# Performance work log

Measured on AMD Instinct MI355X. Metric: run time of the kernel, lower is better.

Reference implementation:

```python
import jax, jax.numpy as jnp
import numpy as np

BS = 128          # batch size (baked into trans_bs = Linear(bs, 1))
SEQ = 100         # raw seq len; InnerComp concat doubles it to 200
D = 64            # user/item embedding dim
HID = 128         # predictor hidden dim
NITEM = 1000000   # item vocab
NNEG = 99         # negative samples (test mode)
TH1 = 0.007       # InnerComp threshold (~1/BS)
TH2 = 0.007       # InterComp threshold


def setup_inputs() -> dict:
    key = jax.random.key(0)
    ks = list(jax.random.split(key, 40))
    def nrm(i, shape, s=0.05):
        return jax.random.normal(ks[i], shape, jnp.float32) * s
    inp = {
        "u_node": jax.random.randint(ks[0], (BS,), 0, NITEM),
        "i_node": jax.random.randint(ks[1], (BS,), 0, NITEM),
        "neg_samples": jax.random.randint(ks[2], (BS, NNEG), 0, NITEM),
        "seq_d1": jax.random.randint(ks[3], (BS, SEQ), 0, NITEM),
        "seq_d2": jax.random.randint(ks[4], (BS, SEQ), 0, NITEM),
        "long_tail_mask_d1": jax.random.randint(ks[5], (BS, SEQ), 0, 2),
        "long_tail_mask_d2": jax.random.randint(ks[6], (BS, SEQ), 0, 2),
        "emb": nrm(7, (NITEM, D)),
    }
    j = 8
    for name in ["inc1", "inc2", "itc1", "itc2"]:
        inp[name + "_Wnn"] = nrm(j, (D, D)); j += 1
        inp[name + "_bnn"] = nrm(j, (D,)); j += 1
        inp[name + "_Wbs"] = nrm(j, (1, BS)); j += 1
        inp[name + "_bbs"] = nrm(j, (1,)); j += 1
    for name in ["gru1", "gru2"]:
        inp[name + "_Wih"] = nrm(j, (3 * D, D)); j += 1
        inp[name + "_Whh"] = nrm(j, (3 * D, D)); j += 1
        inp[name + "_bih"] = nrm(j, (3 * D,)); j += 1
        inp[name + "_bhh"] = nrm(j, (3 * D,)); j += 1
    inp["fc1_W"] = nrm(j, (HID, 2 * D)); j += 1
    inp["fc1_b"] = nrm(j, (HID,)); j += 1
    inp["fc2_W"] = nrm(j, (1, HID)); j += 1
    inp["fc2_b"] = nrm(j, (1,)); j += 1
    return inp


def _comp(seq_self, seq_other, Wnn, bnn, Wbs, bbs, th):
    # Faithful collapse of InnerComp/InterComp: in the torch code,
    # group_bool[i,j] = max(seq_self[j] @ seq_other[j]^T) is independent of i,
    # and so is the trans_bs output. Same math, no O(bs^2 L^2) blowup.
    g = jnp.max(jnp.einsum('bld,bmd->blm', seq_self, seq_other), axis=(1, 2))  # [bs]
    m = (jax.nn.softmax(g) > th).astype(seq_self.dtype)                        # [bs]
    y = (seq_other * m[:, None, None]) @ Wnn.T + bnn                           # [bs,L,d]
    z = jnp.einsum('j,jld->ld', Wbs[0], y) + bbs[0]                            # [L,d]
    z = jnp.broadcast_to(z[None], seq_self.shape)
    return jnp.concatenate([seq_self, z], axis=1)                              # [bs,2L,d]


def _gru(x, Wih, Whh, bih, bhh):
    # torch.nn.GRU, 1 layer, batch_first, h0 = 0. Gate order: r, z, n.
    B, L, _ = x.shape
    H = Whh.shape[1]
    xp = x @ Wih.T + bih  # [B,L,3H] precomputed input projections
    def step(h, xt):
        gh = h @ Whh.T + bhh
        xr, xz, xn = jnp.split(xt, 3, axis=-1)
        hr, hz, hn = jnp.split(gh, 3, axis=-1)
        r = jax.nn.sigmoid(xr + hr)
        z = jax.nn.sigmoid(xz + hz)
        n = jnp.tanh(xn + r * hn)
        hnew = (1 - z) * n + z * h
        return hnew, hnew
    h0 = jnp.zeros((B, H), x.dtype)
    _, hs = jax.lax.scan(step, h0, jnp.swapaxes(xp, 0, 1))
    return jnp.swapaxes(hs, 0, 1)  # [B,L,H]


def reference(u_node, i_node, neg_samples, seq_d1, seq_d2,
              long_tail_mask_d1, long_tail_mask_d2, emb,
              inc1_Wnn, inc1_bnn, inc1_Wbs, inc1_bbs,
              inc2_Wnn, inc2_bnn, inc2_Wbs, inc2_bbs,
              itc1_Wnn, itc1_bnn, itc1_Wbs, itc1_bbs,
              itc2_Wnn, itc2_bnn, itc2_Wbs, itc2_bbs,
              gru1_Wih, gru1_Whh, gru1_bih, gru1_bhh,
              gru2_Wih, gru2_Whh, gru2_bih, gru2_bhh,
              fc1_W, fc1_b, fc2_W, fc2_b):
    i_feat = emb[i_node][:, None, :]     # [bs,1,d]
    neg_feat = emb[neg_samples]          # [bs,99,d]
    s1 = emb[seq_d1]                     # [bs,SEQ,d]
    s2 = emb[seq_d2]
    # InnerComp (self-comparison), doubles seq len
    s1 = _comp(s1, s1, inc1_Wnn, inc1_bnn, inc1_Wbs, inc1_bbs, TH1)
    s2 = _comp(s2, s2, inc2_Wnn, inc2_bnn, inc2_Wbs, inc2_bbs, TH1)
    # GRU per domain
    s1 = _gru(s1, gru1_Wih, gru1_Whh, gru1_bih, gru1_bhh)
    s2 = _gru(s2, gru2_Wih, gru2_Whh, gru2_bih, gru2_bhh)
    # InterComp (cross-domain), doubles seq len again
    s1n = _comp(s1, s2, itc1_Wnn, itc1_bnn, itc1_Wbs, itc1_bbs, TH2)
    s2n = _comp(s2, s1, itc2_Wnn, itc2_bnn, itc2_Wbs, itc2_bbs, TH2)
    u1 = jnp.mean(s1n, axis=1)           # [bs,d]
    u2 = jnp.mean(s2n, axis=1)
    i_all = jnp.concatenate([i_feat, neg_feat], axis=1)  # [bs,100,d]
    def pred(u):
        c = jnp.concatenate([jnp.broadcast_to(u[:, None, :], i_all.shape), i_all], axis=-1)
        h = jax.nn.relu(c @ fc1_W.T + fc1_b)
        return jax.nn.sigmoid(h @ fc2_W.T + fc2_b)[..., 0]  # [bs,100]
    return pred(u1), pred(u2)
```

## Files before the change

kernel.cpp:

```cpp
#include <hip/hip_runtime.h>
#include <hip/hip_bf16.h>
#include <cstdint>
#include <cstddef>

#define TH 0.007f

#define OFF_S1RAW   0u
#define OFF_S2RAW   819200u
#define OFF_IALL    1638400u
#define OFF_GRU1O   2457600u
#define OFF_GRU2O   4096000u
#define OFF_XP1     5734400u
#define OFF_XP2     8192000u
#define OFF_ZP1     10649600u
#define OFF_ZP2     10668800u
#define OFF_ZINC1   10688000u
#define OFF_ZINC2   10694400u
#define OFF_ZITC1   10700800u
#define OFF_ZITC2   10713600u
#define OFF_G3      10726400u
#define OFF_U1      10727300u
#define OFF_U2      10735492u

__device__ __forceinline__ float sigf(float x) { return 1.0f / (1.0f + __expf(-x)); }
__device__ __forceinline__ float tanhf_(float x) { return 1.0f - 2.0f / (__expf(2.0f * x) + 1.0f); }

__global__ void k_gather(const int* __restrict__ i_node, const int* __restrict__ neg,
                         const int* __restrict__ seq1, const int* __restrict__ seq2,
                         const float* __restrict__ emb, float* __restrict__ ws) {
  int tid = threadIdx.x;
  int r = blockIdx.x * 4 + (tid >> 6);
  int d = tid & 63;
  long idx;
  float* dst;
  if (r < 12800) {
    idx = seq1[r];
    dst = ws + OFF_S1RAW + (size_t)r * 64;
  } else if (r < 25600) {
    int rr = r - 12800;
    idx = seq2[rr];
    dst = ws + OFF_S2RAW + (size_t)rr * 64;
  } else {
    int rr = r - 25600;
    int b = rr / 100, i = rr % 100;
    idx = (i == 0) ? i_node[b] : neg[b * 99 + i - 1];
    dst = ws + OFF_IALL + (size_t)rr * 64;
  }
  dst[d] = emb[idx * 64 + d];
}

__global__ __launch_bounds__(256) void k_gmax(const float* __restrict__ A0, const float* __restrict__ B0, float* g0,
                                              const float* __restrict__ A1, const float* __restrict__ B1, float* g1,
                                              int L, int nbhalf) {
  int half = blockIdx.x / nbhalf;
  int b = blockIdx.x % nbhalf;
  const float* A = half ? A1 : A0;
  const float* B = half ? B1 : B0;
  float* gout = half ? g1 : g0;
  __shared__ __align__(16) float SA[64 * 104];
  __shared__ __align__(16) float SB[64 * 104];
  __shared__ float red[4];
  int tid = threadIdx.x;
  int nch = L / 100;
  float gm = -1e30f;
  for (int ai = 0; ai < nch; ++ai) {
    for (int bi = 0; bi < nch; ++bi) {
      __syncthreads();
      for (int e = tid; e < 6400; e += 256) {
        int l = e >> 6, k = e & 63;
        SA[k * 104 + l] = A[((size_t)b * L + ai * 100 + l) * 64 + k];
        SB[k * 104 + l] = B[((size_t)b * L + bi * 100 + l) * 64 + k];
      }
      __syncthreads();
      for (int id = tid; id < 625; id += 256) {
        int ti = id / 25, tj = id % 25;
        int l0 = ti * 4, m0 = tj * 4;
        float acc[4][4];
#pragma unroll
        for (int x = 0; x < 4; ++x)
#pragma unroll
          for (int y = 0; y < 4; ++y) acc[x][y] = 0.0f;
#pragma unroll 16
        for (int k = 0; k < 64; ++k) {
          const float4 av = *reinterpret_cast<const float4*>(&SA[k * 104 + l0]);
          const float4 bv = *reinterpret_cast<const float4*>(&SB[k * 104 + m0]);
          float aa[4] = {av.x, av.y, av.z, av.w};
          float bb[4] = {bv.x, bv.y, bv.z, bv.w};
#pragma unroll
          for (int x = 0; x < 4; ++x)
#pragma unroll
            for (int y = 0; y < 4; ++y) acc[x][y] = fmaf(aa[x], bb[y], acc[x][y]);
        }
        float tm = acc[0][0];
#pragma unroll
        for (int x = 0; x < 4; ++x)
#pragma unroll
          for (int y = 0; y < 4; ++y) tm = fmaxf(tm, acc[x][y]);
        gm = fmaxf(gm, tm);
      }
    }
  }
  for (int off = 32; off; off >>= 1) gm = fmaxf(gm, __shfl_xor(gm, off, 64));
  if ((tid & 63) == 0) red[tid >> 6] = gm;
  __syncthreads();
  if (tid == 0) gout[b] = fmaxf(fmaxf(red[0], red[1]), fmaxf(red[2], red[3]));
}

__global__ void k_z(const float* o0, const float* g0, const float* Wbs0, const float* Wnn0, const float* bnn0, const float* bbs0, float* z0,
                    const float* o1, const float* g1, const float* Wbs1, const float* Wnn1, const float* bnn1, const float* bbs1, float* z1,
                    int L) {
  int comp = blockIdx.x / L;
  int l = blockIdx.x % L;
  const float* other = comp ? o1 : o0;
  const float* g = comp ? g1 : g0;
  const float* Wbs = comp ? Wbs1 : Wbs0;
  const float* Wnn = comp ? Wnn1 : Wnn0;
  const float* bnn = comp ? bnn1 : bnn0;
  const float* bbs = comp ? bbs1 : bbs0;
  float* zout = comp ? z1 : z0;
  int d = threadIdx.x;
  __shared__ float w_s[128];
  __shared__ float tl[64];
  float ga = g[d], gb = g[d + 64];
  float mx = fmaxf(ga, gb);
  for (int off = 32; off; off >>= 1) mx = fmaxf(mx, __shfl_xor(mx, off, 64));
  float ea = __expf(ga - mx), eb = __expf(gb - mx);
  float sm = ea + eb;
  for (int off = 32; off; off >>= 1) sm += __shfl_xor(sm, off, 64);
  float wa = Wbs[d], wb = Wbs[d + 64];
  w_s[d] = (ea / sm > TH) ? wa : 0.0f;
  w_s[d + 64] = (eb / sm > TH) ? wb : 0.0f;
  float cs = wa + wb;
  for (int off = 32; off; off >>= 1) cs += __shfl_xor(cs, off, 64);
  __syncthreads();
  float td = 0.0f;
#pragma unroll 4
  for (int j = 0; j < 128; ++j) td = fmaf(w_s[j], other[((size_t)j * L + l) * 64 + d], td);
  tl[d] = td;
  __syncthreads();
  float acc = fmaf(cs, bnn[d], bbs[0]);
#pragma unroll 8
  for (int k = 0; k < 64; ++k) acc = fmaf(tl[k], Wnn[d * 64 + k], acc);
  zout[l * 64 + d] = acc;
}

__global__ __launch_bounds__(192) void k_xproj(const float* __restrict__ s1raw, const float* __restrict__ s2raw,
                                               const float* __restrict__ zi1, const float* __restrict__ zi2,
                                               const float* __restrict__ W1, const float* __restrict__ b1,
                                               const float* __restrict__ W2, const float* __restrict__ b2,
                                               float* xp1, float* xp2, float* zp1, float* zp2) {
  int blk = blockIdx.x;
  const float* X;
  const float* W;
  const float* bi;
  float* out;
  int nrows, lb;
  if (blk < 800)        { X = s1raw; W = W1; bi = b1; out = xp1; nrows = 12800; lb = blk; }
  else if (blk < 1600)  { X = s2raw; W = W2; bi = b2; out = xp2; nrows = 12800; lb = blk - 800; }
  else if (blk < 1607)  { X = zi1;   W = W1; bi = b1; out = zp1; nrows = 100;   lb = blk - 1600; }
  else                  { X = zi2;   W = W2; bi = b2; out = zp2; nrows = 100;   lb = blk - 1607; }
  int row0 = lb * 16;
  int j = threadIdx.x;
  __shared__ float xt[16 * 64];
  int rmax = nrows - row0;
  if (rmax > 16) rmax = 16;
  int lim = rmax * 64;
  for (int e = j; e < lim; e += 192) xt[e] = X[(size_t)row0 * 64 + e];
  __syncthreads();
  float wreg[64];
#pragma unroll
  for (int k = 0; k < 64; ++k) wreg[k] = W[j * 64 + k];
  float bj = bi[j];
  for (int r = 0; r < rmax; ++r) {
    float acc = bj;
#pragma unroll
    for (int k = 0; k < 64; ++k) acc = fmaf(xt[r * 64 + k], wreg[k], acc);
    out[(size_t)(row0 + r) * 192 + j] = acc;
  }
}

__global__ __launch_bounds__(192) void k_scan(const float* __restrict__ xp1, const float* __restrict__ xp2,
                                              const float* __restrict__ zp1, const float* __restrict__ zp2,
                                              const float* __restrict__ Whh1, const float* __restrict__ bhh1,
                                              const float* __restrict__ Whh2, const float* __restrict__ bhh2,
                                              float* o1, float* o2) {
  int dom = blockIdx.x >> 7;
  int bb = blockIdx.x & 127;
  const float* xp = dom ? xp2 : xp1;
  const float* zp = dom ? zp2 : zp1;
  const float* Whh = dom ? Whh2 : Whh1;
  const float* bhh = dom ? bhh2 : bhh1;
  float* out = (dom ? o2 : o1) + (size_t)bb * 200 * 64;
  int tid = threadIdx.x;
  int g = tid >> 6;
  int i = tid & 63;
  __shared__ __align__(16) float h_s[64];
  __shared__ float r_s[64];
  __shared__ float z_s[64];
  float w[64];
  const float* wrow = Whh + (size_t)(g * 64 + i) * 64;
#pragma unroll
  for (int k4 = 0; k4 < 16; ++k4) {
    float4 wv = *reinterpret_cast<const float4*>(wrow + 4 * k4);
    w[4 * k4 + 0] = wv.x; w[4 * k4 + 1] = wv.y; w[4 * k4 + 2] = wv.z; w[4 * k4 + 3] = wv.w;
  }
  float bg = bhh[g * 64 + i];
  if (tid < 64) h_s[tid] = 0.0f;
  float h_i = 0.0f;
  float x_cur = xp[((size_t)bb * 100) * 192 + g * 64 + i];
  __syncthreads();
  for (int t = 0; t < 200; ++t) {
    float x_nxt = 0.0f;
    if (t < 199) {
      const float* pn = (t < 99) ? xp + ((size_t)bb * 100 + t + 1) * 192
                                 : zp + (size_t)(t + 1 - 100) * 192;
      x_nxt = pn[g * 64 + i];
    }
    float a0 = bg, a1 = 0.0f, a2 = 0.0f, a3 = 0.0f;
#pragma unroll
    for (int k4 = 0; k4 < 16; ++k4) {
      float4 hv = *reinterpret_cast<const float4*>(&h_s[4 * k4]);
      a0 = fmaf(hv.x, w[4 * k4 + 0], a0);
      a1 = fmaf(hv.y, w[4 * k4 + 1], a1);
      a2 = fmaf(hv.z, w[4 * k4 + 2], a2);
      a3 = fmaf(hv.w, w[4 * k4 + 3], a3);
    }
    float a = (a0 + a1) + (a2 + a3);
    if (g == 0)      r_s[i] = sigf(x_cur + a);
    else if (g == 1) z_s[i] = sigf(x_cur + a);
    __syncthreads();
    if (g == 2) {
      float r = r_s[i], z = z_s[i];
      float n = tanhf_(x_cur + r * a);
      h_i = n + z * (h_i - n);
      h_s[i] = h_i;
      out[t * 64 + i] = h_i;
    }
    __syncthreads();
    x_cur = x_nxt;
  }
}

__global__ void k_mean(const float* g1o, const float* g2o,
                       const float* zi1, const float* zi2,
                       float* u1, float* u2) {
  int dom = blockIdx.x >> 7, bb = blockIdx.x & 127, d = threadIdx.x;
  const float* s = dom ? g2o : g1o;
  const float* z = dom ? zi2 : zi1;
  float* u = dom ? u2 : u1;
  float acc = 0.0f;
  const float* sp = s + (size_t)bb * 200 * 64 + d;
#pragma unroll 4
  for (int t = 0; t < 200; ++t) acc += sp[t * 64];
#pragma unroll 4
  for (int l = 0; l < 200; ++l) acc += z[l * 64 + d];
  u[bb * 64 + d] = acc * 0.0025f;
}

__global__ __launch_bounds__(256) void k_pred(const float* __restrict__ u1, const float* __restrict__ u2,
                                              const float* __restrict__ iall,
                                              const float* __restrict__ W1, const float* __restrict__ b1v,
                                              const float* __restrict__ w2v, const float* __restrict__ b2v,
                                              float* __restrict__ outp) {
  int p = blockIdx.x >> 7, bb = blockIdx.x & 127;
  const float* u = (p ? u2 : u1) + bb * 64;
  int tid = threadIdx.x;
  int lane = tid & 63;
  int jh = (tid >> 6) & 1;
  int ih = tid >> 7;
  int i = ih * 64 + lane;
  bool act = i < 100;
  __shared__ float aU[128];
  __shared__ float part[2][100];
  if (tid < 128) {
    int j = tid;
    float acc = b1v[j];
#pragma unroll 8
    for (int k = 0; k < 64; ++k) acc = fmaf(u[k], W1[j * 128 + k], acc);
    aU[j] = acc;
  }
  float V[64];
  const float* vp = iall + ((size_t)bb * 100 + (act ? i : 0)) * 64;
#pragma unroll
  for (int k4 = 0; k4 < 16; ++k4) {
    float4 vv = *reinterpret_cast<const float4*>(vp + 4 * k4);
    V[4 * k4 + 0] = vv.x; V[4 * k4 + 1] = vv.y; V[4 * k4 + 2] = vv.z; V[4 * k4 + 3] = vv.w;
  }
  __syncthreads();
  float acc_o = 0.0f;
  for (int j = jh * 64; j < jh * 64 + 64; ++j) {
    const float* wrow = W1 + j * 128 + 64;
    float d0 = aU[j], d1 = 0.0f, d2 = 0.0f, d3 = 0.0f;
#pragma unroll
    for (int k = 0; k < 16; ++k) {
      d0 = fmaf(V[4 * k + 0], wrow[4 * k + 0], d0);
      d1 = fmaf(V[4 * k + 1], wrow[4 * k + 1], d1);
      d2 = fmaf(V[4 * k + 2], wrow[4 * k + 2], d2);
      d3 = fmaf(V[4 * k + 3], wrow[4 * k + 3], d3);
    }
    float hrelu = fmaxf((d0 + d1) + (d2 + d3), 0.0f);
    acc_o = fmaf(w2v[j], hrelu, acc_o);
  }
  if (act) part[jh][i] = acc_o;
  __syncthreads();
  if (act && jh == 0) {
    float s = part[0][i] + part[1][i] + b2v[0];
    outp[(size_t)p * 12800 + bb * 100 + i] = 1.0f / (1.0f + __expf(-s));
  }
}

extern "C" void kernel_launch(void* const* d_in, const int* in_sizes, int n_in,
                              void* d_out, int out_size, void* d_ws, size_t ws_size,
                              hipStream_t stream) {
  const int* i_node = (const int*)d_in[1];
  const int* neg = (const int*)d_in[2];
  const int* seq1 = (const int*)d_in[3];
  const int* seq2 = (const int*)d_in[4];
  const float* emb = (const float*)d_in[7];
  const float* inc1_Wnn = (const float*)d_in[8];
  const float* inc1_bnn = (const float*)d_in[9];
  const float* inc1_Wbs = (const float*)d_in[10];
  const float* inc1_bbs = (const float*)d_in[11];
  const float* inc2_Wnn = (const float*)d_in[12];
  const float* inc2_bnn = (const float*)d_in[13];
  const float* inc2_Wbs = (const float*)d_in[14];
  const float* inc2_bbs = (const float*)d_in[15];
  const float* itc1_Wnn = (const float*)d_in[16];
  const float* itc1_bnn = (const float*)d_in[17];
  const float* itc1_Wbs = (const float*)d_in[18];
  const float* itc1_bbs = (const float*)d_in[19];
  const float* itc2_Wnn = (const float*)d_in[20];
  const float* itc2_bnn = (const float*)d_in[21];
  const float* itc2_Wbs = (const float*)d_in[22];
  const float* itc2_bbs = (const float*)d_in[23];
  const float* gru1_Wih = (const float*)d_in[24];
  const float* gru1_Whh = (const float*)d_in[25];
  const float* gru1_bih = (const float*)d_in[26];
  const float* gru1_bhh = (const float*)d_in[27];
  const float* gru2_Wih = (const float*)d_in[28];
  const float* gru2_Whh = (const float*)d_in[29];
  const float* gru2_bih = (const float*)d_in[30];
  const float* gru2_bhh = (const float*)d_in[31];
  const float* fc1_W = (const float*)d_in[32];
  const float* fc1_b = (const float*)d_in[33];
  const float* fc2_W = (const float*)d_in[34];
  const float* fc2_b = (const float*)d_in[35];

  float* ws = (float*)d_ws;
  float* out = (float*)d_out;
  float* s1raw = ws + OFF_S1RAW;
  float* s2raw = ws + OFF_S2RAW;
  float* iall = ws + OFF_IALL;
  float* gru1o = ws + OFF_GRU1O;
  float* gru2o = ws + OFF_GRU2O;
  float* xp1 = ws + OFF_XP1;
  float* xp2 = ws + OFF_XP2;
  float* zp1 = ws + OFF_ZP1;
  float* zp2 = ws + OFF_ZP2;
  float* zinc1 = ws + OFF_ZINC1;
  float* zinc2 = ws + OFF_ZINC2;
  float* zitc1 = ws + OFF_ZITC1;
  float* zitc2 = ws + OFF_ZITC2;
  float* g3 = ws + OFF_G3;
  float* u1 = ws + OFF_U1;
  float* u2 = ws + OFF_U2;

  k_gather<<<9600, 256, 0, stream>>>(i_node, neg, seq1, seq2, emb, ws);
  k_gmax<<<256, 256, 0, stream>>>(s1raw, s1raw, g3, s2raw, s2raw, g3 + 128, 100, 128);
  k_z<<<200, 64, 0, stream>>>(s1raw, g3, inc1_Wbs, inc1_Wnn, inc1_bnn, inc1_bbs, zinc1,
                              s2raw, g3 + 128, inc2_Wbs, inc2_Wnn, inc2_bnn, inc2_bbs, zinc2, 100);
  k_xproj<<<1614, 192, 0, stream>>>(s1raw, s2raw, zinc1, zinc2,
                                    gru1_Wih, gru1_bih, gru2_Wih, gru2_bih,
                                    xp1, xp2, zp1, zp2);
  k_scan<<<256, 192, 0, stream>>>(xp1, xp2, zp1, zp2, gru1_Whh, gru1_bhh, gru2_Whh, gru2_bhh,
                                  gru1o, gru2o);
  k_gmax<<<128, 256, 0, stream>>>(gru1o, gru2o, g3 + 256, gru1o, gru2o, g3 + 256, 200, 128);
  k_z<<<400, 64, 0, stream>>>(gru2o, g3 + 256, itc1_Wbs, itc1_Wnn, itc1_bnn, itc1_bbs, zitc1,
                              gru1o, g3 + 256, itc2_Wbs, itc2_Wnn, itc2_bnn, itc2_bbs, zitc2, 200);
  k_mean<<<256, 64, 0, stream>>>(gru1o, gru2o, zitc1, zitc2, u1, u2);
  k_pred<<<256, 256, 0, stream>>>(u1, u2, iall, fc1_W, fc1_b, fc2_W, fc2_b, out);
}
```

Baseline: 698.0 us.

## Run GRU scan in one wavefront, fuse mean and item gather into prediction

The GRU recurrent scan now uses a single 64-thread wavefront per sequence. Each thread computes all three gates, with the r-gate weights held in registers and the z/n weights in swizzled shared memory. This removes the two block-wide barriers per timestep that the three-wave version needed. Separately, the mean-pooling kernel and the item/negative embedding gather are folded into the prediction kernel, which drops a launch and a workspace round trip. The risks are that the serial per-step FMA work per thread triples, and that the code relies on implicit wavefront lockstep for h_s with no barrier.

```diff
diff --git a/kernel.cpp b/kernel.cpp
--- a/kernel.cpp
+++ b/kernel.cpp
@@ -7,7 +7,6 @@
 
 #define OFF_S1RAW   0u
 #define OFF_S2RAW   819200u
-#define OFF_IALL    1638400u
 #define OFF_GRU1O   2457600u
 #define OFF_GRU2O   4096000u
 #define OFF_XP1     5734400u
@@ -19,14 +18,11 @@
 #define OFF_ZITC1   10700800u
 #define OFF_ZITC2   10713600u
 #define OFF_G3      10726400u
-#define OFF_U1      10727300u
-#define OFF_U2      10735492u
 
 __device__ __forceinline__ float sigf(float x) { return 1.0f / (1.0f + __expf(-x)); }
 __device__ __forceinline__ float tanhf_(float x) { return 1.0f - 2.0f / (__expf(2.0f * x) + 1.0f); }
 
-__global__ void k_gather(const int* __restrict__ i_node, const int* __restrict__ neg,
-                         const int* __restrict__ seq1, const int* __restrict__ seq2,
+__global__ void k_gather(const int* __restrict__ seq1, const int* __restrict__ seq2,
                          const float* __restrict__ emb, float* __restrict__ ws) {
   int tid = threadIdx.x;
   int r = blockIdx.x * 4 + (tid >> 6);
@@ -36,15 +32,10 @@
   if (r < 12800) {
     idx = seq1[r];
     dst = ws + OFF_S1RAW + (size_t)r * 64;
-  } else if (r < 25600) {
+  } else {
     int rr = r - 12800;
     idx = seq2[rr];
     dst = ws + OFF_S2RAW + (size_t)rr * 64;
-  } else {
-    int rr = r - 25600;
-    int b = rr / 100, i = rr % 100;
-    idx = (i == 0) ? i_node[b] : neg[b * 99 + i - 1];
-    dst = ws + OFF_IALL + (size_t)rr * 64;
   }
   dst[d] = emb[idx * 64 + d];
 }
@@ -179,11 +170,14 @@
   }
 }
 
-__global__ __launch_bounds__(192) void k_scan(const float* __restrict__ xp1, const float* __restrict__ xp2,
-                                              const float* __restrict__ zp1, const float* __restrict__ zp2,
-                                              const float* __restrict__ Whh1, const float* __restrict__ bhh1,
-                                              const float* __restrict__ Whh2, const float* __restrict__ bhh2,
-                                              float* o1, float* o2) {
+__device__ __forceinline__ int swz(int row, int k4) {
+  return row * 64 + ((k4 * 4) ^ ((row & 7) * 4));
+}
+__global__ __launch_bounds__(64, 1) void k_scan(const float* __restrict__ xp1, const float* __restrict__ xp2,
+                                                const float* __restrict__ zp1, const float* __restrict__ zp2,
+                                                const float* __restrict__ Whh1, const float* __restrict__ bhh1,
+                                                const float* __restrict__ Whh2, const float* __restrict__ bhh2,
+                                                float* o1, float* o2) {
   int dom = blockIdx.x >> 7;
   int bb = blockIdx.x & 127;
   const float* xp = dom ? xp2 : xp1;
@@ -191,96 +185,97 @@
   const float* Whh = dom ? Whh2 : Whh1;
   const float* bhh = dom ? bhh2 : bhh1;
   float* out = (dom ? o2 : o1) + (size_t)bb * 200 * 64;
-  int tid = threadIdx.x;
-  int g = tid >> 6;
-  int i = tid & 63;
+  int i = threadIdx.x;
+  __shared__ __align__(16) float wz_s[64 * 64];
+  __shared__ __align__(16) float wn_s[64 * 64];
   __shared__ __align__(16) float h_s[64];
-  __shared__ float r_s[64];
-  __shared__ float z_s[64];
-  float w[64];
-  const float* wrow = Whh + (size_t)(g * 64 + i) * 64;
+  float4 wr4[16];
 #pragma unroll
   for (int k4 = 0; k4 < 16; ++k4) {
-    float4 wv = *reinterpret_cast<const float4*>(wrow + 4 * k4);
-    w[4 * k4 + 0] = wv.x; w[4 * k4 + 1] = wv.y; w[4 * k4 + 2] = wv.z; w[4 * k4 + 3] = wv.w;
-  }
-  float bg = bhh[g * 64 + i];
-  if (tid < 64) h_s[tid] = 0.0f;
-  float h_i = 0.0f;
-  float x_cur = xp[((size_t)bb * 100) * 192 + g * 64 + i];
-  __syncthreads();
+    wr4[k4] = *reinterpret_cast<const float4*>(Whh + (size_t)i * 64 + k4 * 4);
+    *reinterpret_cast<float4*>(&wz_s[swz(i, k4)]) =
+        *reinterpret_cast<const float4*>(Whh + (size_t)(64 + i) * 64 + k4 * 4);
+    *reinterpret_cast<float4*>(&wn_s[swz(i, k4)]) =
+        *reinterpret_cast<const float4*>(Whh + (size_t)(128 + i) * 64 + k4 * 4);
+  }
+  float br = bhh[i], bz = bhh[64 + i], bn = bhh[128 + i];
+  float h = 0.0f;
+  h_s[i] = 0.0f;
+  const float* p0 = xp + (size_t)bb * 100 * 192;
+  float xr = p0[i], xz = p0[64 + i], xn = p0[128 + i];
   for (int t = 0; t < 200; ++t) {
-    float x_nxt = 0.0f;
+    float nxr = 0.f, nxz = 0.f, nxn = 0.f;
     if (t < 199) {
       const float* pn = (t < 99) ? xp + ((size_t)bb * 100 + t + 1) * 192
                                  : zp + (size_t)(t + 1 - 100) * 192;
-      x_nxt = pn[g * 64 + i];
+      nxr = pn[i]; nxz = pn[64 + i]; nxn = pn[128 + i];
     }
-    float a0 = bg, a1 = 0.0f, a2 = 0.0f, a3 = 0.0f;
+    float ar0 = br, ar1 = 0.f, az0 = bz, az1 = 0.f, an0 = bn, an1 = 0.f;
 #pragma unroll
     for (int k4 = 0; k4 < 16; ++k4) {
-      float4 hv = *reinterpret_cast<const float4*>(&h_s[4 * k4]);
-      a0 = fmaf(hv.x, w[4 * k4 + 0], a0);
-      a1 = fmaf(hv.y, w[4 * k4 + 1], a1);
-      a2 = fmaf(hv.z, w[4 * k4 + 2], a2);
-      a3 = fmaf(hv.w, w[4 * k4 + 3], a3);
+      const float4 hv = *reinterpret_cast<const float4*>(&h_s[k4 * 4]);
+      const float4 zv = *reinterpret_cast<const float4*>(&wz_s[swz(i, k4)]);
+      const float4 nv = *reinterpret_cast<const float4*>(&wn_s[swz(i, k4)]);
+      ar0 = fmaf(hv.x, wr4[k4].x, ar0); ar1 = fmaf(hv.y, wr4[k4].y, ar1);
+      ar0 = fmaf(hv.z, wr4[k4].z, ar0); ar1 = fmaf(hv.w, wr4[k4].w, ar1);
+      az0 = fmaf(hv.x, zv.x, az0);      az1 = fmaf(hv.y, zv.y, az1);
+      az0 = fmaf(hv.z, zv.z, az0);      az1 = fmaf(hv.w, zv.w, az1);
+      an0 = fmaf(hv.x, nv.x, an0);      an1 = fmaf(hv.y, nv.y, an1);
+      an0 = fmaf(hv.z, nv.z, an0);      an1 = fmaf(hv.w, nv.w, an1);
     }
-    float a = (a0 + a1) + (a2 + a3);
-    if (g == 0)      r_s[i] = sigf(x_cur + a);
-    else if (g == 1) z_s[i] = sigf(x_cur + a);
-    __syncthreads();
-    if (g == 2) {
-      float r = r_s[i], z = z_s[i];
-      float n = tanhf_(x_cur + r * a);
-      h_i = n + z * (h_i - n);
-      h_s[i] = h_i;
-      out[t * 64 + i] = h_i;
-    }
-    __syncthreads();
-    x_cur = x_nxt;
-  }
-}
-
-__global__ void k_mean(const float* g1o, const float* g2o,
-                       const float* zi1, const float* zi2,
-                       float* u1, float* u2) {
-  int dom = blockIdx.x >> 7, bb = blockIdx.x & 127, d = threadIdx.x;
-  const float* s = dom ? g2o : g1o;
-  const float* z = dom ? zi2 : zi1;
-  float* u = dom ? u2 : u1;
-  float acc = 0.0f;
-  const float* sp = s + (size_t)bb * 200 * 64 + d;
-#pragma unroll 4
-  for (int t = 0; t < 200; ++t) acc += sp[t * 64];
-#pragma unroll 4
-  for (int l = 0; l < 200; ++l) acc += z[l * 64 + d];
-  u[bb * 64 + d] = acc * 0.0025f;
-}
-
-__global__ __launch_bounds__(256) void k_pred(const float* __restrict__ u1, const float* __restrict__ u2,
-                                              const float* __restrict__ iall,
+    float r = sigf(xr + ar0 + ar1);
+    float z = sigf(xz + az0 + az1);
+    float n = tanhf_(xn + r * (an0 + an1));
+    h = n + z * (h - n);
+    out[t * 64 + i] = h;
+    h_s[i] = h;
+    xr = nxr; xz = nxz; xn = nxn;
+  }
+}
+
+__global__ __launch_bounds__(256) void k_pred(const float* __restrict__ g1o, const float* __restrict__ g2o,
+                                              const float* __restrict__ zi1, const float* __restrict__ zi2,
+                                              const int* __restrict__ i_node, const int* __restrict__ neg,
+                                              const float* __restrict__ emb,
                                               const float* __restrict__ W1, const float* __restrict__ b1v,
                                               const float* __restrict__ w2v, const float* __restrict__ b2v,
                                               float* __restrict__ outp) {
   int p = blockIdx.x >> 7, bb = blockIdx.x & 127;
-  const float* u = (p ? u2 : u1) + bb * 64;
+  const float* s = p ? g2o : g1o;
+  const float* zz = p ? zi2 : zi1;
   int tid = threadIdx.x;
+  __shared__ float up[4][64];
+  __shared__ float u_s[64];
+  __shared__ float aU[128];
+  __shared__ float part[2][100];
+  {
+    int d = tid & 63, c = tid >> 6;
+    float acc = 0.0f;
+    const float* sp = s + (size_t)bb * 12800 + c * 50 * 64 + d;
+#pragma unroll 2
+    for (int t = 0; t < 50; ++t) acc += sp[t * 64];
+    const float* zp = zz + c * 50 * 64 + d;
+#pragma unroll 2
+    for (int t = 0; t < 50; ++t) acc += zp[t * 64];
+    up[c][d] = acc;
+  }
+  __syncthreads();
+  if (tid < 64) u_s[tid] = (up[0][tid] + up[1][tid] + up[2][tid] + up[3][tid]) * 0.0025f;
+  __syncthreads();
+  if (tid < 128) {
+    float acc = b1v[tid];
+#pragma unroll 8
+    for (int k = 0; k < 64; ++k) acc = fmaf(u_s[k], W1[tid * 128 + k], acc);
+    aU[tid] = acc;
+  }
   int lane = tid & 63;
   int jh = (tid >> 6) & 1;
   int ih = tid >> 7;
   int i = ih * 64 + lane;
   bool act = i < 100;
-  __shared__ float aU[128];
-  __shared__ float part[2][100];
-  if (tid < 128) {
-    int j = tid;
-    float acc = b1v[j];
-#pragma unroll 8
-    for (int k = 0; k < 64; ++k) acc = fmaf(u[k], W1[j * 128 + k], acc);
-    aU[j] = acc;
-  }
+  long idx = act ? (long)((i == 0) ? i_node[bb] : neg[bb * 99 + i - 1]) : 0;
   float V[64];
-  const float* vp = iall + ((size_t)bb * 100 + (act ? i : 0)) * 64;
+  const float* vp = emb + (size_t)idx * 64;
 #pragma unroll
   for (int k4 = 0; k4 < 16; ++k4) {
     float4 vv = *reinterpret_cast<const float4*>(vp + 4 * k4);
@@ -304,8 +299,8 @@
   if (act) part[jh][i] = acc_o;
   __syncthreads();
   if (act && jh == 0) {
-    float s = part[0][i] + part[1][i] + b2v[0];
-    outp[(size_t)p * 12800 + bb * 100 + i] = 1.0f / (1.0f + __expf(-s));
+    float sres = part[0][i] + part[1][i] + b2v[0];
+    outp[(size_t)p * 12800 + bb * 100 + i] = 1.0f / (1.0f + __expf(-sres));
   }
 }
 
@@ -350,7 +345,6 @@
   float* out = (float*)d_out;
   float* s1raw = ws + OFF_S1RAW;
   float* s2raw = ws + OFF_S2RAW;
-  float* iall = ws + OFF_IALL;
   float* gru1o = ws + OFF_GRU1O;
   float* gru2o = ws + OFF_GRU2O;
   float* xp1 = ws + OFF_XP1;
@@ -362,21 +356,19 @@
   float* zitc1 = ws + OFF_ZITC1;
   float* zitc2 = ws + OFF_ZITC2;
   float* g3 = ws + OFF_G3;
-  float* u1 = ws + OFF_U1;
-  float* u2 = ws + OFF_U2;
-
-  k_gather<<<9600, 256, 0, stream>>>(i_node, neg, seq1, seq2, emb, ws);
+
+  k_gather<<<6400, 256, 0, stream>>>(seq1, seq2, emb, ws);
   k_gmax<<<256, 256, 0, stream>>>(s1raw, s1raw, g3, s2raw, s2raw, g3 + 128, 100, 128);
   k_z<<<200, 64, 0, stream>>>(s1raw, g3, inc1_Wbs, inc1_Wnn, inc1_bnn, inc1_bbs, zinc1,
                               s2raw, g3 + 128, inc2_Wbs, inc2_Wnn, inc2_bnn, inc2_bbs, zinc2, 100);
   k_xproj<<<1614, 192, 0, stream>>>(s1raw, s2raw, zinc1, zinc2,
                                     gru1_Wih, gru1_bih, gru2_Wih, gru2_bih,
                                     xp1, xp2, zp1, zp2);
-  k_scan<<<256, 192, 0, stream>>>(xp1, xp2, zp1, zp2, gru1_Whh, gru1_bhh, gru2_Whh, gru2_bhh,
-                                  gru1o, gru2o);
+  k_scan<<<256, 64, 0, stream>>>(xp1, xp2, zp1, zp2, gru1_Whh, gru1_bhh, gru2_Whh, gru2_bhh,
+                                 gru1o, gru2o);
   k_gmax<<<128, 256, 0, stream>>>(gru1o, gru2o, g3 + 256, gru1o, gru2o, g3 + 256, 200, 128);
   k_z<<<400, 64, 0, stream>>>(gru2o, g3 + 256, itc1_Wbs, itc1_Wnn, itc1_bnn, itc1_bbs, zitc1,
                               gru1o, g3 + 256, itc2_Wbs, itc2_Wnn, itc2_bnn, itc2_bbs, zitc2, 200);
-  k_mean<<<256, 64, 0, stream>>>(gru1o, gru2o, zitc1, zitc2, u1, u2);
-  k_pred<<<256, 256, 0, stream>>>(u1, u2, iall, fc1_W, fc1_b, fc2_W, fc2_b, out);
-}
+  k_pred<<<256, 256, 0, stream>>>(gru1o, gru2o, zitc1, zitc2, i_node, neg, emb,
+                                  fc1_W, fc1_b, fc2_W, fc2_b, out);
+}
```

Measured after the change: 700.7 us. No clear change (+0.4%).
